# Kernel optimization log

Hardware: AMD Instinct MI355X
Metric: run time of the kernel (lower is better)

The kernel has to match this reference:

```python
import jax, jax.numpy as jnp
import numpy as np

EPS = 1e-06

def setup_inputs() -> dict:
    key = jax.random.key(0)
    k1, k2, k3, k4 = jax.random.split(key, 4)
    N, E, D = 100000, 1600000, 128
    feat = jax.random.normal(k1, (N, D), dtype=jnp.float32)
    src = jax.random.randint(k2, (E,), 0, N, dtype=jnp.int32)
    dst = jax.random.randint(k3, (E,), 0, N, dtype=jnp.int32)
    W = jax.random.normal(k4, (D, D), dtype=jnp.float32) * 0.05
    b = jnp.zeros((D,), dtype=jnp.float32)
    a2 = jnp.ones((D,), dtype=jnp.float32)
    b2 = jnp.zeros((D,), dtype=jnp.float32)
    return {"feat": feat, "src": src, "dst": dst, "W": W, "b": b, "a2": a2, "b2": b2}

def reference(feat, src, dst, W, b, a2, b2):
    N, D = feat.shape
    # LayerNorm (torch std is unbiased, eps added to std, not var)
    mean = jnp.mean(feat, axis=-1, keepdims=True)
    std = jnp.std(feat, axis=-1, keepdims=True, ddof=1)
    h = a2 * (feat - mean) / (std + EPS) + b2
    # DGL GraphConv, norm='both': D_out^{-1/2} gather-sum D_in^{-1/2}, then W, b, relu
    ones = jnp.ones(src.shape[0], dtype=feat.dtype)
    out_deg = jax.ops.segment_sum(ones, src, num_segments=N)
    in_deg = jax.ops.segment_sum(ones, dst, num_segments=N)
    norm_out = jax.lax.rsqrt(jnp.maximum(out_deg, 1.0))[:, None]
    norm_in = jax.lax.rsqrt(jnp.maximum(in_deg, 1.0))[:, None]
    h = h * norm_out
    # in_feats == out_feats -> DGL multiplies weight first
    h = h @ W
    agg = jax.ops.segment_sum(h[src], dst, num_segments=N)  # [N, D]
    rst = agg * norm_in + b
    rst = jax.nn.relu(rst)
    # residual (Identity since in_feats == out_feats); dropout is identity at eval
    return rst + feat
```

## Files before the change

kernel.cpp:

```cpp
#include <hip/hip_runtime.h>

#define D 128
#define BSH 6
#define BN 64
#define NBUK_MAX 2048
#define NBLK 256
#define SRT_CAP 2048
#define NW_LDS 25600

typedef __bf16 bf16x8 __attribute__((ext_vector_type(8)));
typedef float  f32x4  __attribute__((ext_vector_type(4)));

__device__ __forceinline__ unsigned short f2bf(float f) {
    unsigned u = __float_as_uint(f);
    unsigned r = (u + 0x7FFF + ((u >> 16) & 1)) >> 16;
    return (unsigned short)r;
}
__device__ __forceinline__ float bf2f(unsigned short s) {
    return __uint_as_float(((unsigned)s) << 16);
}

__global__ __launch_bounds__(256) void wpack_kernel(const float* __restrict__ W,
        unsigned short* __restrict__ Wp) {
    int idx = blockIdx.x * 256 + threadIdx.x;
    int k = idx >> 7;
    int c = idx & 127;
    Wp[c * D + (k ^ ((c & 7) << 3))] = f2bf(W[idx]);
}

__global__ __launch_bounds__(1024) void count_kernel(const int* __restrict__ src,
        const int* __restrict__ dst, int* __restrict__ hist,
        unsigned* __restrict__ partial, int E, int nbuk, int chunk, int NW) {
    __shared__ unsigned ph[NW_LDS];
    __shared__ int hb[NBUK_MAX];
    int t = threadIdx.x;
    for (int i = t; i < NW_LDS; i += 1024) ph[i] = 0;
    for (int i = t; i < nbuk; i += 1024) hb[i] = 0;
    __syncthreads();
    int lo = blockIdx.x * chunk;
    int hi = min(E, lo + chunk);
    for (int e = lo + t; e < hi; e += 1024) {
        int s = src[e], d = dst[e];
        atomicAdd(&ph[s >> 2], 1u << ((s & 3) * 8));
        atomicAdd(&hb[d >> BSH], 1);
    }
    __syncthreads();
    int* hrow = hist + (size_t)blockIdx.x * nbuk;
    for (int i = t; i < nbuk; i += 1024) hrow[i] = hb[i];
    unsigned* prow = partial + (size_t)blockIdx.x * NW;
    for (int i = t; i < NW; i += 1024) prow[i] = ph[i];
}

__global__ __launch_bounds__(1024) void reduce_kernel(const unsigned* __restrict__ partial,
        unsigned* __restrict__ podeg, int NW) {
    __shared__ unsigned acc[16][64];
    int t = threadIdx.x;
    int wl = t & 63, bg = t >> 6;
    int w = blockIdx.x * 64 + wl;
    unsigned s = 0;
    if (w < NW) {
        for (int b = bg; b < NBLK; b += 16) s += partial[(size_t)b * NW + w];
    }
    acc[bg][wl] = s;
    __syncthreads();
    if (bg == 0 && w < NW) {
        unsigned tot = 0;
        #pragma unroll
        for (int g = 0; g < 16; ++g) tot += acc[g][wl];
        podeg[w] = tot;
    }
}

__global__ __launch_bounds__(64) void hscan_kernel(int* __restrict__ hist,
        int* __restrict__ colsum, int nbuk) {
    int buk = blockIdx.x;
    int l = threadIdx.x;
    int v[4]; int s = 0;
    #pragma unroll
    for (int i = 0; i < 4; ++i) {
        v[i] = hist[(size_t)(l * 4 + i) * nbuk + buk];
        s += v[i];
    }
    int x = s;
    #pragma unroll
    for (int m = 1; m < 64; m <<= 1) {
        int y = __shfl_up(x, m);
        if (l >= m) x += y;
    }
    int base = x - s;
    #pragma unroll
    for (int i = 0; i < 4; ++i) {
        int tmp = v[i];
        hist[(size_t)(l * 4 + i) * nbuk + buk] = base;
        base += tmp;
    }
    if (l == 63) colsum[buk] = x;
}

__global__ __launch_bounds__(1024) void bscan_kernel(const int* __restrict__ colsum,
        int* __restrict__ base, int nbuk, int E) {
    __shared__ int s[1024];
    int t = threadIdx.x;
    int i0 = 2 * t, i1 = 2 * t + 1;
    int a = (i0 < nbuk) ? colsum[i0] : 0;
    int c = (i1 < nbuk) ? colsum[i1] : 0;
    int p = a + c;
    s[t] = p;
    __syncthreads();
    #pragma unroll
    for (int off = 1; off < 1024; off <<= 1) {
        int x = (t >= off) ? s[t - off] : 0;
        __syncthreads();
        s[t] += x;
        __syncthreads();
    }
    int ex = s[t] - p;
    if (i0 < nbuk) base[i0] = ex;
    if (i1 < nbuk) base[i1] = ex + a;
    if (t == 0) base[nbuk] = E;
}

__global__ __launch_bounds__(1024) void scatter_kernel(const int* __restrict__ src,
        const int* __restrict__ dst, const int* __restrict__ hist,
        const int* __restrict__ base, unsigned* __restrict__ pairs,
        int E, int nbuk, int chunk) {
    __shared__ int cur[NBUK_MAX];
    int t = threadIdx.x;
    const int* hrow = hist + (size_t)blockIdx.x * nbuk;
    for (int i = t; i < nbuk; i += 1024) cur[i] = base[i] + hrow[i];
    __syncthreads();
    int lo = blockIdx.x * chunk;
    int hi = min(E, lo + chunk);
    for (int e = lo + t; e < hi; e += 1024) {
        int d = dst[e];
        int pos = atomicAdd(&cur[d >> BSH], 1);
        pairs[pos] = ((unsigned)(d & (BN - 1)) << 24) | (unsigned)src[e];
    }
}

__global__ __launch_bounds__(256) void ln_gemm_kernel(const float* __restrict__ feat,
        const unsigned short* __restrict__ Wp, const float* __restrict__ a2,
        const float* __restrict__ b2, const unsigned* __restrict__ podeg,
        unsigned short* __restrict__ hw, int N) {
    __shared__ unsigned short Wt[D * D];
    __shared__ unsigned short hs[64 * D];

    const int t = threadIdx.x;
    const int base = blockIdx.x * 64;

    {
        const uint4* Wp4 = (const uint4*)Wp;
        uint4* Wl4 = (uint4*)Wt;
        #pragma unroll
        for (int i = 0; i < 8; ++i) Wl4[i * 256 + t] = Wp4[i * 256 + t];
    }

    {
        const int r = t >> 2;
        const int sub = t & 3;
        const int grow = base + r;
        const bool valid = grow < N;

        float4 v[8];
        float sum = 0.f, sumsq = 0.f;
        if (valid) {
            const float4* fr = (const float4*)(feat + (size_t)grow * D + sub * 32);
            #pragma unroll
            for (int i = 0; i < 8; ++i) {
                v[i] = fr[i];
                sum   += v[i].x + v[i].y + v[i].z + v[i].w;
                sumsq += v[i].x * v[i].x + v[i].y * v[i].y + v[i].z * v[i].z + v[i].w * v[i].w;
            }
        }
        sum   += __shfl_xor(sum, 1);   sumsq += __shfl_xor(sumsq, 1);
        sum   += __shfl_xor(sum, 2);   sumsq += __shfl_xor(sumsq, 2);

        if (valid) {
            float mean = sum * (1.f / 128.f);
            float var  = fmaxf((sumsq - 128.f * mean * mean) * (1.f / 127.f), 0.f);
            float inv  = 1.f / (sqrtf(var) + 1e-6f);
            int   od   = (podeg[grow >> 2] >> ((grow & 3) * 8)) & 0xFF;
            float norm = rsqrtf(fmaxf((float)od, 1.f));
            float sa   = inv * norm;
            #pragma unroll
            for (int i = 0; i < 8; ++i) {
                int c0 = sub * 32 + i * 4;
                float4 av = *(const float4*)&a2[c0];
                float4 bv = *(const float4*)&b2[c0];
                ushort4 o;
                o.x = f2bf(av.x * (v[i].x - mean) * sa + bv.x * norm);
                o.y = f2bf(av.y * (v[i].y - mean) * sa + bv.y * norm);
                o.z = f2bf(av.z * (v[i].z - mean) * sa + bv.z * norm);
                o.w = f2bf(av.w * (v[i].w - mean) * sa + bv.w * norm);
                *(ushort4*)&hs[r * D + (c0 ^ ((r & 7) << 3))] = o;
            }
        } else {
            ushort4 z = make_ushort4(0, 0, 0, 0);
            #pragma unroll
            for (int i = 0; i < 8; ++i) {
                int c0 = sub * 32 + i * 4;
                *(ushort4*)&hs[r * D + (c0 ^ ((r & 7) << 3))] = z;
            }
        }
    }
    __syncthreads();

    {
        const int w = t >> 6;
        const int l = t & 63;
        const int lrow = l & 15;
        const int kg = l >> 4;
        const int arow = w * 16 + lrow;

        bf16x8 a[4];
        #pragma unroll
        for (int kt = 0; kt < 4; ++kt) {
            int col = kt * 32 + kg * 8;
            a[kt] = *reinterpret_cast<const bf16x8*>(&hs[arow * D + (col ^ ((arow & 7) << 3))]);
        }

        f32x4 acc[8];
        #pragma unroll
        for (int ct = 0; ct < 8; ++ct) acc[ct] = (f32x4){0.f, 0.f, 0.f, 0.f};

        #pragma unroll
        for (int ct = 0; ct < 8; ++ct) {
            int brow = ct * 16 + lrow;
            #pragma unroll
            for (int kt = 0; kt < 4; ++kt) {
                int col = kt * 32 + kg * 8;
                bf16x8 bfr = *reinterpret_cast<const bf16x8*>(&Wt[brow * D + (col ^ ((brow & 7) << 3))]);
                acc[ct] = __builtin_amdgcn_mfma_f32_16x16x32_bf16(a[kt], bfr, acc[ct], 0, 0, 0);
            }
        }

        #pragma unroll
        for (int ct = 0; ct < 8; ++ct) {
            #pragma unroll
            for (int p = 0; p < 4; ++p) {
                int gr = base + w * 16 + kg * 4 + p;
                if (gr < N) hw[(size_t)gr * D + ct * 16 + lrow] = f2bf(acc[ct][p]);
            }
        }
    }
}

__global__ __launch_bounds__(512) void gather_kernel(const unsigned* __restrict__ pairs,
        const int* __restrict__ bukbase, const unsigned short* __restrict__ hw,
        const float* __restrict__ feat, const float* __restrict__ bias,
        float* __restrict__ out, int N) {
    __shared__ unsigned srt[SRT_CAP];
    __shared__ int cnt[BN];
    __shared__ int ofs[BN + 1];

    int t = threadIdx.x;
    int buk = blockIdx.x;
    int beg = bukbase[buk];
    int ne = bukbase[buk + 1] - beg;
    if (ne > SRT_CAP) ne = SRT_CAP;

    if (t < BN) cnt[t] = 0;
    __syncthreads();

    for (int i = t; i < ne; i += 512)
        atomicAdd(&cnt[pairs[beg + i] >> 24], 1);
    __syncthreads();

    if (t < BN) {
        int c = cnt[t];
        int x = c;
        #pragma unroll
        for (int m = 1; m < BN; m <<= 1) {
            int y = __shfl_up(x, m);
            if (t >= m) x += y;
        }
        ofs[t] = x - c;
        if (t == BN - 1) ofs[BN] = x;
        cnt[t] = x - c;
    }
    __syncthreads();

    for (int i = t; i < ne; i += 512) {
        unsigned p = pairs[beg + i];
        int pos = atomicAdd(&cnt[p >> 24], 1);
        srt[pos] = p & 0xFFFFFFu;
    }
    __syncthreads();

    int wv = t >> 6;
    int lane = t & 63;
    int half = lane >> 5;
    int l32 = lane & 31;
    int co = l32 * 4;

    for (int nl = wv; nl < BN; nl += 8) {
        int n = (buk << BSH) + nl;
        if (n >= N) break;
        int s0 = ofs[nl], s1 = ofs[nl + 1];
        int deg = s1 - s0;

        float a0 = 0.f, a1 = 0.f, a2v = 0.f, a3 = 0.f;
        int e = s0 + half;
        for (; e + 6 < s1; e += 8) {
            int x0 = srt[e], x1 = srt[e + 2], x2 = srt[e + 4], x3 = srt[e + 6];
            ushort4 q0 = *(const ushort4*)&hw[(size_t)x0 * D + co];
            ushort4 q1 = *(const ushort4*)&hw[(size_t)x1 * D + co];
            ushort4 q2 = *(const ushort4*)&hw[(size_t)x2 * D + co];
            ushort4 q3 = *(const ushort4*)&hw[(size_t)x3 * D + co];
            a0  += bf2f(q0.x) + bf2f(q1.x) + bf2f(q2.x) + bf2f(q3.x);
            a1  += bf2f(q0.y) + bf2f(q1.y) + bf2f(q2.y) + bf2f(q3.y);
            a2v += bf2f(q0.z) + bf2f(q1.z) + bf2f(q2.z) + bf2f(q3.z);
            a3  += bf2f(q0.w) + bf2f(q1.w) + bf2f(q2.w) + bf2f(q3.w);
        }
        for (; e < s1; e += 2) {
            int x0 = srt[e];
            ushort4 q0 = *(const ushort4*)&hw[(size_t)x0 * D + co];
            a0  += bf2f(q0.x);
            a1  += bf2f(q0.y);
            a2v += bf2f(q0.z);
            a3  += bf2f(q0.w);
        }

        a0  += __shfl_xor(a0, 32);
        a1  += __shfl_xor(a1, 32);
        a2v += __shfl_xor(a2v, 32);
        a3  += __shfl_xor(a3, 32);

        if (half == 0) {
            float ni = rsqrtf(fmaxf((float)deg, 1.f));
            float4 bb = *(const float4*)&bias[co];
            float4 f  = *(const float4*)&feat[(size_t)n * D + co];
            float4 o;
            o.x = fmaxf(fmaf(a0,  ni, bb.x), 0.f) + f.x;
            o.y = fmaxf(fmaf(a1,  ni, bb.y), 0.f) + f.y;
            o.z = fmaxf(fmaf(a2v, ni, bb.z), 0.f) + f.z;
            o.w = fmaxf(fmaf(a3,  ni, bb.w), 0.f) + f.w;
            *(float4*)&out[(size_t)n * D + co] = o;
        }
    }
}

extern "C" void kernel_launch(void* const* d_in, const int* in_sizes, int n_in,
                              void* d_out, int out_size, void* d_ws, size_t ws_size,
                              hipStream_t stream) {
    const float* feat = (const float*)d_in[0];
    const int*   src  = (const int*)d_in[1];
    const int*   dst  = (const int*)d_in[2];
    const float* W    = (const float*)d_in[3];
    const float* b    = (const float*)d_in[4];
    const float* a2   = (const float*)d_in[5];
    const float* b2   = (const float*)d_in[6];

    const int N = in_sizes[0] / D;
    const int E = in_sizes[1];
    const int NW = (N + 3) / 4;
    const int nbuk = (N + BN - 1) >> BSH;
    const int chunk = (E + NBLK - 1) / NBLK;

    float* out = (float*)d_out;

    unsigned short* hw = (unsigned short*)d_ws;
    unsigned* podeg = (unsigned*)(hw + (size_t)N * D);
    int* hist    = (int*)(podeg + NW);
    int* colsum  = hist + (size_t)NBLK * NBUK_MAX;
    int* bukbase = colsum + NBUK_MAX;
    unsigned short* Wp = (unsigned short*)(bukbase + (NBUK_MAX + 1));
    unsigned* pairs = (unsigned*)(Wp + D * D);
    unsigned* partial = pairs + E;

    wpack_kernel<<<64, 256, 0, stream>>>(W, Wp);
    count_kernel<<<NBLK, 1024, 0, stream>>>(src, dst, hist, partial, E, nbuk, chunk, NW);
    reduce_kernel<<<(NW + 63) / 64, 1024, 0, stream>>>(partial, podeg, NW);
    hscan_kernel<<<nbuk, 64, 0, stream>>>(hist, colsum, nbuk);
    bscan_kernel<<<1, 1024, 0, stream>>>(colsum, bukbase, nbuk, E);
    scatter_kernel<<<NBLK, 1024, 0, stream>>>(src, dst, hist, bukbase, pairs, E, nbuk, chunk);

    ln_gemm_kernel<<<(N + 63) / 64, 256, 0, stream>>>(feat, Wp, a2, b2, podeg, hw, N);

    gather_kernel<<<nbuk, 512, 0, stream>>>(pairs, bukbase, hw, feat, b, out, N);
}
```

Measured before the change: 151.8 us.

## Merge preprocessing kernels and co-schedule scatter with LayerNorm-GEMM

Folds the weight packing into count_kernel, merges the degree reduction and the histogram column scan into one launch, and runs the edge scatter and the LayerNorm+GEMM in a single kernel whose block ranges handle each job. The goal is fewer launches and letting the scatter overlap the dense GEMM work. The GEMM blocks now take 128 rows with 512 threads and read W fragments straight from global memory (relying on cache) instead of staging W in LDS. That raises global traffic per MFMA and makes the hist-scan blocks idle 960 of 1024 threads.

```diff
diff --git a/kernel.cpp b/kernel.cpp
--- a/kernel.cpp
+++ b/kernel.cpp
@@ -20,20 +20,21 @@
     return __uint_as_float(((unsigned)s) << 16);
 }
 
-__global__ __launch_bounds__(256) void wpack_kernel(const float* __restrict__ W,
-        unsigned short* __restrict__ Wp) {
-    int idx = blockIdx.x * 256 + threadIdx.x;
-    int k = idx >> 7;
-    int c = idx & 127;
-    Wp[c * D + (k ^ ((c & 7) << 3))] = f2bf(W[idx]);
-}
-
 __global__ __launch_bounds__(1024) void count_kernel(const int* __restrict__ src,
-        const int* __restrict__ dst, int* __restrict__ hist,
+        const int* __restrict__ dst, const float* __restrict__ W,
+        unsigned short* __restrict__ Wp, int* __restrict__ hist,
         unsigned* __restrict__ partial, int E, int nbuk, int chunk, int NW) {
     __shared__ unsigned ph[NW_LDS];
     __shared__ int hb[NBUK_MAX];
     int t = threadIdx.x;
+
+    if (blockIdx.x < 16) {
+        int idx = blockIdx.x * 1024 + t;
+        int k = idx >> 7;
+        int c = idx & 127;
+        Wp[c * D + (k ^ ((c & 7) << 3))] = f2bf(W[idx]);
+    }
+
     for (int i = t; i < NW_LDS; i += 1024) ph[i] = 0;
     for (int i = t; i < nbuk; i += 1024) hb[i] = 0;
     __syncthreads();
@@ -51,50 +52,52 @@
     for (int i = t; i < NW; i += 1024) prow[i] = ph[i];
 }
 
-__global__ __launch_bounds__(1024) void reduce_kernel(const unsigned* __restrict__ partial,
-        unsigned* __restrict__ podeg, int NW) {
-    __shared__ unsigned acc[16][64];
-    int t = threadIdx.x;
-    int wl = t & 63, bg = t >> 6;
-    int w = blockIdx.x * 64 + wl;
-    unsigned s = 0;
-    if (w < NW) {
-        for (int b = bg; b < NBLK; b += 16) s += partial[(size_t)b * NW + w];
-    }
-    acc[bg][wl] = s;
-    __syncthreads();
-    if (bg == 0 && w < NW) {
-        unsigned tot = 0;
-        #pragma unroll
-        for (int g = 0; g < 16; ++g) tot += acc[g][wl];
-        podeg[w] = tot;
-    }
-}
-
-__global__ __launch_bounds__(64) void hscan_kernel(int* __restrict__ hist,
-        int* __restrict__ colsum, int nbuk) {
-    int buk = blockIdx.x;
-    int l = threadIdx.x;
-    int v[4]; int s = 0;
-    #pragma unroll
-    for (int i = 0; i < 4; ++i) {
-        v[i] = hist[(size_t)(l * 4 + i) * nbuk + buk];
-        s += v[i];
-    }
-    int x = s;
-    #pragma unroll
-    for (int m = 1; m < 64; m <<= 1) {
-        int y = __shfl_up(x, m);
-        if (l >= m) x += y;
-    }
-    int base = x - s;
-    #pragma unroll
-    for (int i = 0; i < 4; ++i) {
-        int tmp = v[i];
-        hist[(size_t)(l * 4 + i) * nbuk + buk] = base;
-        base += tmp;
-    }
-    if (l == 63) colsum[buk] = x;
+__global__ __launch_bounds__(1024) void rh_kernel(const unsigned* __restrict__ partial,
+        unsigned* __restrict__ podeg, int NW, int nrb,
+        int* __restrict__ hist, int* __restrict__ colsum, int nbuk) {
+    if ((int)blockIdx.x < nrb) {
+        __shared__ unsigned acc[16][64];
+        int t = threadIdx.x;
+        int wl = t & 63, bg = t >> 6;
+        int w = blockIdx.x * 64 + wl;
+        unsigned s = 0;
+        if (w < NW) {
+            for (int b = bg; b < NBLK; b += 16) s += partial[(size_t)b * NW + w];
+        }
+        acc[bg][wl] = s;
+        __syncthreads();
+        if (bg == 0 && w < NW) {
+            unsigned tot = 0;
+            #pragma unroll
+            for (int g = 0; g < 16; ++g) tot += acc[g][wl];
+            podeg[w] = tot;
+        }
+    } else {
+        int buk = blockIdx.x - nrb;
+        int l = threadIdx.x;
+        if (l < 64 && buk < nbuk) {
+            int v[4]; int s = 0;
+            #pragma unroll
+            for (int i = 0; i < 4; ++i) {
+                v[i] = hist[(size_t)(l * 4 + i) * nbuk + buk];
+                s += v[i];
+            }
+            int x = s;
+            #pragma unroll
+            for (int m = 1; m < 64; m <<= 1) {
+                int y = __shfl_up(x, m);
+                if (l >= m) x += y;
+            }
+            int base = x - s;
+            #pragma unroll
+            for (int i = 0; i < 4; ++i) {
+                int tmp = v[i];
+                hist[(size_t)(l * 4 + i) * nbuk + buk] = base;
+                base += tmp;
+            }
+            if (l == 63) colsum[buk] = x;
+        }
+    }
 }
 
 __global__ __launch_bounds__(1024) void bscan_kernel(const int* __restrict__ colsum,
@@ -120,45 +123,40 @@
     if (t == 0) base[nbuk] = E;
 }
 
-__global__ __launch_bounds__(1024) void scatter_kernel(const int* __restrict__ src,
+__global__ __launch_bounds__(512) void mid_kernel(const int* __restrict__ src,
         const int* __restrict__ dst, const int* __restrict__ hist,
         const int* __restrict__ base, unsigned* __restrict__ pairs,
-        int E, int nbuk, int chunk) {
-    __shared__ int cur[NBUK_MAX];
-    int t = threadIdx.x;
-    const int* hrow = hist + (size_t)blockIdx.x * nbuk;
-    for (int i = t; i < nbuk; i += 1024) cur[i] = base[i] + hrow[i];
-    __syncthreads();
-    int lo = blockIdx.x * chunk;
-    int hi = min(E, lo + chunk);
-    for (int e = lo + t; e < hi; e += 1024) {
-        int d = dst[e];
-        int pos = atomicAdd(&cur[d >> BSH], 1);
-        pairs[pos] = ((unsigned)(d & (BN - 1)) << 24) | (unsigned)src[e];
-    }
-}
-
-__global__ __launch_bounds__(256) void ln_gemm_kernel(const float* __restrict__ feat,
-        const unsigned short* __restrict__ Wp, const float* __restrict__ a2,
-        const float* __restrict__ b2, const unsigned* __restrict__ podeg,
-        unsigned short* __restrict__ hw, int N) {
-    __shared__ unsigned short Wt[D * D];
-    __shared__ unsigned short hs[64 * D];
+        int E, int nbuk, int chunk,
+        const float* __restrict__ feat, const unsigned short* __restrict__ Wp,
+        const float* __restrict__ a2, const float* __restrict__ b2,
+        const unsigned* __restrict__ podeg, unsigned short* __restrict__ hw, int N) {
+    __shared__ union {
+        int cur[NBUK_MAX];
+        unsigned short hs[128 * D];
+    } u;
 
     const int t = threadIdx.x;
-    const int base = blockIdx.x * 64;
-
-    {
-        const uint4* Wp4 = (const uint4*)Wp;
-        uint4* Wl4 = (uint4*)Wt;
-        #pragma unroll
-        for (int i = 0; i < 8; ++i) Wl4[i * 256 + t] = Wp4[i * 256 + t];
-    }
+
+    if ((int)blockIdx.x < NBLK) {
+        const int* hrow = hist + (size_t)blockIdx.x * nbuk;
+        for (int i = t; i < nbuk; i += 512) u.cur[i] = base[i] + hrow[i];
+        __syncthreads();
+        int lo = blockIdx.x * chunk;
+        int hi = min(E, lo + chunk);
+        for (int e = lo + t; e < hi; e += 512) {
+            int d = dst[e];
+            int pos = atomicAdd(&u.cur[d >> BSH], 1);
+            pairs[pos] = ((unsigned)(d & (BN - 1)) << 24) | (unsigned)src[e];
+        }
+        return;
+    }
+
+    const int rbase = (blockIdx.x - NBLK) * 128;
 
     {
         const int r = t >> 2;
         const int sub = t & 3;
-        const int grow = base + r;
+        const int grow = rbase + r;
         const bool valid = grow < N;
 
         float4 v[8];
@@ -192,14 +190,14 @@
                 o.y = f2bf(av.y * (v[i].y - mean) * sa + bv.y * norm);
                 o.z = f2bf(av.z * (v[i].z - mean) * sa + bv.z * norm);
                 o.w = f2bf(av.w * (v[i].w - mean) * sa + bv.w * norm);
-                *(ushort4*)&hs[r * D + (c0 ^ ((r & 7) << 3))] = o;
+                *(ushort4*)&u.hs[r * D + (c0 ^ ((r & 7) << 3))] = o;
             }
         } else {
             ushort4 z = make_ushort4(0, 0, 0, 0);
             #pragma unroll
             for (int i = 0; i < 8; ++i) {
                 int c0 = sub * 32 + i * 4;
-                *(ushort4*)&hs[r * D + (c0 ^ ((r & 7) << 3))] = z;
+                *(ushort4*)&u.hs[r * D + (c0 ^ ((r & 7) << 3))] = z;
             }
         }
     }
@@ -216,7 +214,7 @@
         #pragma unroll
         for (int kt = 0; kt < 4; ++kt) {
             int col = kt * 32 + kg * 8;
-            a[kt] = *reinterpret_cast<const bf16x8*>(&hs[arow * D + (col ^ ((arow & 7) << 3))]);
+            a[kt] = *reinterpret_cast<const bf16x8*>(&u.hs[arow * D + (col ^ ((arow & 7) << 3))]);
         }
 
         f32x4 acc[8];
@@ -229,7 +227,7 @@
             #pragma unroll
             for (int kt = 0; kt < 4; ++kt) {
                 int col = kt * 32 + kg * 8;
-                bf16x8 bfr = *reinterpret_cast<const bf16x8*>(&Wt[brow * D + (col ^ ((brow & 7) << 3))]);
+                bf16x8 bfr = *reinterpret_cast<const bf16x8*>(&Wp[brow * D + (col ^ ((brow & 7) << 3))]);
                 acc[ct] = __builtin_amdgcn_mfma_f32_16x16x32_bf16(a[kt], bfr, acc[ct], 0, 0, 0);
             }
         }
@@ -238,7 +236,7 @@
         for (int ct = 0; ct < 8; ++ct) {
             #pragma unroll
             for (int p = 0; p < 4; ++p) {
-                int gr = base + w * 16 + kg * 4 + p;
+                int gr = rbase + w * 16 + kg * 4 + p;
                 if (gr < N) hw[(size_t)gr * D + ct * 16 + lrow] = f2bf(acc[ct][p]);
             }
         }
@@ -356,6 +354,8 @@
     const int NW = (N + 3) / 4;
     const int nbuk = (N + BN - 1) >> BSH;
     const int chunk = (E + NBLK - 1) / NBLK;
+    const int nrb = (NW + 63) / 64;
+    const int nln = (N + 127) / 128;
 
     float* out = (float*)d_out;
 
@@ -368,14 +368,10 @@
     unsigned* pairs = (unsigned*)(Wp + D * D);
     unsigned* partial = pairs + E;
 
-    wpack_kernel<<<64, 256, 0, stream>>>(W, Wp);
-    count_kernel<<<NBLK, 1024, 0, stream>>>(src, dst, hist, partial, E, nbuk, chunk, NW);
-    reduce_kernel<<<(NW + 63) / 64, 1024, 0, stream>>>(partial, podeg, NW);
-    hscan_kernel<<<nbuk, 64, 0, stream>>>(hist, colsum, nbuk);
+    count_kernel<<<NBLK, 1024, 0, stream>>>(src, dst, W, Wp, hist, partial, E, nbuk, chunk, NW);
+    rh_kernel<<<nrb + nbuk, 1024, 0, stream>>>(partial, podeg, NW, nrb, hist, colsum, nbuk);
     bscan_kernel<<<1, 1024, 0, stream>>>(colsum, bukbase, nbuk, E);
-    scatter_kernel<<<NBLK, 1024, 0, stream>>>(src, dst, hist, bukbase, pairs, E, nbuk, chunk);
-
-    ln_gemm_kernel<<<(N + 63) / 64, 256, 0, stream>>>(feat, Wp, a2, b2, podeg, hw, N);
-
+    mid_kernel<<<NBLK + nln, 512, 0, stream>>>(src, dst, hist, bukbase, pairs, E, nbuk, chunk,
+                                               feat, Wp, a2, b2, podeg, hw, N);
     gather_kernel<<<nbuk, 512, 0, stream>>>(pairs, bukbase, hw, feat, b, out, N);
 }
```

Result: no change. 152.0 us (+0.1%).
